# Kernel optimization log

Hardware: AMD Instinct MI355X
Metric: run time of the kernel (lower is better)

Reference implementation:

```python
import jax, jax.numpy as jnp
import numpy as np

NUM_HEADS = 16
HEAD_DIM = 128
HIDDEN = NUM_HEADS * HEAD_DIM


def rotate_half(x):
    x1, x2 = jnp.split(x, 2, axis=-1)
    return jnp.concatenate((-x2, x1), axis=-1)


def setup_inputs() -> dict:
    key = jax.random.key(0)
    ks = jax.random.split(key, 7)
    b, s = 2, 2048
    return {
        "hidden_states": jax.random.normal(ks[0], (b, s, HIDDEN), dtype=jnp.float32),
        "cos": jax.random.normal(ks[1], (1, 1, s, HEAD_DIM), dtype=jnp.float32),
        "sin": jax.random.normal(ks[2], (1, 1, s, HEAD_DIM), dtype=jnp.float32),
        "Wq": jax.random.normal(ks[3], (HIDDEN, HIDDEN), dtype=jnp.float32) * 0.02,
        "Wk": jax.random.normal(ks[4], (HIDDEN, HIDDEN), dtype=jnp.float32) * 0.02,
        "Wv": jax.random.normal(ks[5], (HIDDEN, HIDDEN), dtype=jnp.float32) * 0.02,
        "Wo": jax.random.normal(ks[6], (HIDDEN, HIDDEN), dtype=jnp.float32) * 0.02,
    }


def reference(hidden_states, cos, sin, Wq, Wk, Wv, Wo):
    b, s, _ = hidden_states.shape

    def proj(W):
        # [b,s,hidden] -> [b,H,s,D]
        return (hidden_states @ W).reshape(b, s, NUM_HEADS, HEAD_DIM).transpose(0, 2, 1, 3)

    q = proj(Wq)
    k = proj(Wk)
    v = proj(Wv)

    # RoPE: cos/sin [1,1,s,D] broadcast over batch and heads
    q = q * cos + rotate_half(q) * sin
    k = k * cos + rotate_half(k) * sin

    scale = 1.0 / jnp.sqrt(jnp.asarray(HEAD_DIM, dtype=q.dtype))
    scores = jnp.einsum("bhqd,bhkd->bhqk", q, k) * scale  # [b,H,s,s]
    attn = jax.nn.softmax(scores, axis=-1)  # no mask applied (matches source)
    out = jnp.einsum("bhqk,bhkd->bhqd", attn, v)  # [b,H,s,D]
    out = out.transpose(0, 2, 1, 3).reshape(b, s, HIDDEN)
    return out @ Wo
```

## Files before the change

### kernel.cpp

```cpp
#include <hip/hip_runtime.h>

typedef short bf16x8 __attribute__((ext_vector_type(8)));
typedef float f32x4 __attribute__((ext_vector_type(4)));

#define HID   2048
#define S_LEN 2048
#define NH    16
#define HD    128
#define BATCH 2
#define NROWS (BATCH * S_LEN)

__device__ __forceinline__ float bf2f(unsigned short u) {
    union { unsigned int i; float f; } v;
    v.i = ((unsigned int)u) << 16;
    return v.f;
}
__device__ __forceinline__ unsigned short f2bf(float f) {
    union { float f; unsigned int i; } v;
    v.f = f;
    unsigned int u = v.i;
    return (unsigned short)((u + 0x7fffu + ((u >> 16) & 1u)) >> 16);
}

__device__ __forceinline__ unsigned int pkbf(float a, float b) {
#if defined(__has_builtin) && __has_builtin(__builtin_amdgcn_cvt_pk_bf16_f32)
    typedef __bf16 bf2_t __attribute__((ext_vector_type(2)));
    bf2_t v = __builtin_amdgcn_cvt_pk_bf16_f32(a, b);
    unsigned int u;
    __builtin_memcpy(&u, &v, 4);
    return u;
#else
    return (unsigned int)f2bf(a) | ((unsigned int)f2bf(b) << 16);
#endif
}

__device__ __forceinline__ float exp2_fast(float x) {
#if defined(__has_builtin) && __has_builtin(__builtin_amdgcn_exp2f)
    return __builtin_amdgcn_exp2f(x);
#else
    return __expf(x * 0.6931471805599453f);
#endif
}

__device__ __forceinline__ void async16(const unsigned short* g, unsigned short* l) {
    __builtin_amdgcn_global_load_lds(
        (const __attribute__((address_space(1))) unsigned int*)g,
        (__attribute__((address_space(3))) unsigned int*)l, 16, 0, 0);
}

__global__ __launch_bounds__(256) void prep(const float* __restrict__ hs,
                                            const float* __restrict__ Wa,
                                            const float* __restrict__ Wb,
                                            const float* __restrict__ Wc,
                                            unsigned short* __restrict__ Xb,
                                            unsigned short* __restrict__ WT) {
    int z = blockIdx.z;
    int t = threadIdx.x;
    if (z == 3) {
        size_t idx = (((size_t)blockIdx.y * 64 + blockIdx.x) * 256 + t) * 8;
        float4 v0 = *(const float4*)(hs + idx);
        float4 v1 = *(const float4*)(hs + idx + 4);
        uint4 o;
        o.x = pkbf(v0.x, v0.y);
        o.y = pkbf(v0.z, v0.w);
        o.z = pkbf(v1.x, v1.y);
        o.w = pkbf(v1.z, v1.w);
        *(uint4*)(Xb + idx) = o;
        return;
    }
    __shared__ float tile[32][33];
    int tx = t & 31, ty = t >> 5;
    int bx = blockIdx.x, by = blockIdx.y;
    const float* W = (z == 0) ? Wa : ((z == 1) ? Wb : Wc);
    unsigned short* dst = WT + (size_t)z * HID * HID;
#pragma unroll
    for (int i = 0; i < 4; i++)
        tile[ty + i * 8][tx] = W[(size_t)(by * 32 + ty + i * 8) * HID + bx * 32 + tx];
    __syncthreads();
#pragma unroll
    for (int i = 0; i < 4; i++)
        dst[(size_t)(bx * 32 + ty + i * 8) * HID + by * 32 + tx] = f2bf(tile[tx][ty + i * 8]);
}

__global__ __launch_bounds__(256) void transpose_cast(const float* __restrict__ W,
                                                      unsigned short* __restrict__ WT) {
    __shared__ float tile[32][33];
    int t = threadIdx.x;
    int tx = t & 31, ty = t >> 5;
    int bx = blockIdx.x, by = blockIdx.y;
#pragma unroll
    for (int i = 0; i < 4; i++)
        tile[ty + i * 8][tx] = W[(size_t)(by * 32 + ty + i * 8) * HID + bx * 32 + tx];
    __syncthreads();
#pragma unroll
    for (int i = 0; i < 4; i++)
        WT[(size_t)(bx * 32 + ty + i * 8) * HID + by * 32 + tx] = f2bf(tile[tx][ty + i * 8]);
}

template <int MODE>
__global__ __launch_bounds__(256, 2) void gemm_bt(const unsigned short* __restrict__ A,
                                                  const unsigned short* __restrict__ Bt,
                                                  unsigned short* __restrict__ Qo,
                                                  unsigned short* __restrict__ Ko,
                                                  unsigned short* __restrict__ Vo,
                                                  float* __restrict__ Fo,
                                                  const float* __restrict__ cosp,
                                                  const float* __restrict__ sinp,
                                                  int n_shift) {
    __shared__ unsigned short SM[16384];
    unsigned short* Asm = SM;
    unsigned short* Bsm = SM + 8192;
    int t = threadIdx.x;
    int wave = t >> 6, lane = t & 63;
    int wm = wave >> 1, wn = wave & 1;
    int c = lane & 15, quad = lane >> 4;
    int m0 = blockIdx.y * 128, nloc = blockIdx.x * 128;

    int lr = lane >> 3;
    int cb = (lane & 7) ^ (lr & 7);
    const unsigned short* Ag = A + (size_t)(m0 + wave * 32 + lr) * HID + cb * 8;
    const unsigned short* Bg = Bt + (size_t)(nloc + wave * 32 + lr) * HID + cb * 8;
    unsigned short* Al = Asm + wave * 2048;
    unsigned short* Bl = Bsm + wave * 2048;

    f32x4 zero = {0.f, 0.f, 0.f, 0.f};
    f32x4 acc[4][4];
#pragma unroll
    for (int i = 0; i < 4; i++)
#pragma unroll
        for (int j = 0; j < 4; j++) acc[i][j] = zero;

    for (int it = 0; it < 32; it++) {
        int k0 = it * 64;
#pragma unroll
        for (int j = 0; j < 4; j++) {
            async16(Ag + k0 + j * 8 * HID, Al + j * 512);
            async16(Bg + k0 + j * 8 * HID, Bl + j * 512);
        }
        __syncthreads();
#pragma unroll
        for (int kk = 0; kk < 2; kk++) {
            bf16x8 af[4], bfr[4];
#pragma unroll
            for (int mt = 0; mt < 4; mt++)
                af[mt] = *(const bf16x8*)(Asm + (wm * 64 + mt * 16 + c) * 64 +
                                          (((kk * 4 + quad) ^ (c & 7)) * 8));
#pragma unroll
            for (int nt = 0; nt < 4; nt++)
                bfr[nt] = *(const bf16x8*)(Bsm + (wn * 64 + nt * 16 + c) * 64 +
                                           (((kk * 4 + quad) ^ (c & 7)) * 8));
#pragma unroll
            for (int mt = 0; mt < 4; mt++)
#pragma unroll
                for (int nt = 0; nt < 4; nt++)
                    acc[mt][nt] = __builtin_amdgcn_mfma_f32_16x16x32_bf16(af[mt], bfr[nt],
                                                                          acc[mt][nt], 0, 0, 0);
        }
        __syncthreads();
    }

    if (MODE == 2) {
#pragma unroll
        for (int mt = 0; mt < 4; mt++)
#pragma unroll
            for (int nt = 0; nt < 4; nt++)
#pragma unroll
                for (int r = 0; r < 4; r++) {
                    int row = m0 + wm * 64 + mt * 16 + quad * 4 + r;
                    int col = nloc + wn * 64 + nt * 16 + c;
                    Fo[(size_t)row * HID + col] = acc[mt][nt][r];
                }
    } else {
        int nglob0 = n_shift + nloc;
        int mat = nglob0 >> 11;
        int h = (nglob0 & 2047) >> 7;
        if (mat == 2) {
#pragma unroll
            for (int mt = 0; mt < 4; mt++)
#pragma unroll
                for (int nt = 0; nt < 4; nt++) {
                    int d = wn * 64 + nt * 16 + c;
                    int row0 = m0 + wm * 64 + mt * 16 + quad * 4;
                    int b = row0 >> 11, s = row0 & 2047;
                    ushort4 o;
                    o.x = f2bf(acc[mt][nt][0]);
                    o.y = f2bf(acc[mt][nt][1]);
                    o.z = f2bf(acc[mt][nt][2]);
                    o.w = f2bf(acc[mt][nt][3]);
                    *(ushort4*)(Vo + ((size_t)(b * NH + h) * HD + d) * S_LEN + s) = o;
                }
        } else {
            unsigned short* Cb = (mat == 0) ? Qo : Ko;
            float scl = (mat == 0) ? 0.12751743f : 1.0f;
            __syncthreads();
#pragma unroll
            for (int mt = 0; mt < 4; mt++)
#pragma unroll
                for (int nt = 0; nt < 4; nt++) {
                    ushort4 o;
                    o.x = f2bf(acc[mt][nt][0]);
                    o.y = f2bf(acc[mt][nt][1]);
                    o.z = f2bf(acc[mt][nt][2]);
                    o.w = f2bf(acc[mt][nt][3]);
                    *(ushort4*)(SM + (mt * 4 + nt) * 1024 + t * 4) = o;
                }
            __syncthreads();
            int partner = (wm * 2 + (wn ^ 1)) * 64 + lane;
            float sgn = wn ? 1.0f : -1.0f;
#pragma unroll
            for (int mt = 0; mt < 4; mt++) {
#pragma unroll
                for (int nt = 0; nt < 4; nt++) {
                    ushort4 pv = *(const ushort4*)(SM + (mt * 4 + nt) * 1024 + partner * 4);
                    float part[4] = {bf2f(pv.x), bf2f(pv.y), bf2f(pv.z), bf2f(pv.w)};
                    int col = wn * 64 + nt * 16 + c;
#pragma unroll
                    for (int r = 0; r < 4; r++) {
                        int row = m0 + wm * 64 + mt * 16 + quad * 4 + r;
                        int b = row >> 11, s = row & 2047;
                        float cv = cosp[s * HD + col], sv = sinp[s * HD + col];
                        float out = (acc[mt][nt][r] * cv + sgn * part[r] * sv) * scl;
                        Cb[((size_t)(b * NH + h) * S_LEN + s) * HD + col] = f2bf(out);
                    }
                }
            }
        }
    }
}

#define PKS 72
__global__ __launch_bounds__(256, 2) void attn_kernel(const unsigned short* __restrict__ Q,
                                                      const unsigned short* __restrict__ Kg,
                                                      const unsigned short* __restrict__ Vt,
                                                      unsigned short* __restrict__ Aout) {
    __shared__ unsigned short Ksm[2 * 64 * 128];
    __shared__ unsigned short Vsm[128 * 64];
    __shared__ __align__(16) unsigned short Psm[4 * 2 * 16 * PKS];
    int bh = blockIdx.y;
    int b = bh >> 4, h = bh & 15;
    int t = threadIdx.x;
    int wave = t >> 6, lane = t & 63;
    int c = lane & 15, quad = lane >> 4;
    int q0 = blockIdx.x * 128 + wave * 32;
    const unsigned short* Qp = Q + (size_t)bh * S_LEN * HD;
    const unsigned short* Kp = Kg + (size_t)bh * S_LEN * HD;
    const unsigned short* Vp = Vt + (size_t)bh * HD * S_LEN;

    bf16x8 qf[2][4];
#pragma unroll
    for (int qn = 0; qn < 2; qn++)
#pragma unroll
        for (int kk = 0; kk < 4; kk++)
            qf[qn][kk] = *(const bf16x8*)(Qp + (size_t)(q0 + qn * 16 + c) * HD + kk * 32 + quad * 8);

    f32x4 zero = {0.f, 0.f, 0.f, 0.f};
    f32x4 o_acc[2][8];
#pragma unroll
    for (int qn = 0; qn < 2; qn++)
#pragma unroll
        for (int nt = 0; nt < 8; nt++) o_acc[qn][nt] = zero;
    float lsum[2] = {0.f, 0.f};

#define STAGE_K(CH, BUF) {                                                      \
    _Pragma("unroll")                                                           \
    for (int j = 0; j < 4; j++) {                                               \
        int fc = (wave * 4 + j) * 64 + lane;                                    \
        int rK = fc >> 4, cbK = (fc & 15) ^ (rK & 15);                          \
        async16(Kp + (size_t)((CH) * 64 + rK) * HD + cbK * 8,                   \
                Ksm + (BUF) * 8192 + (wave * 4 + j) * 512); } }
#define STAGE_V(CH) {                                                           \
    _Pragma("unroll")                                                           \
    for (int j = 0; j < 4; j++) {                                               \
        int fc = (wave * 4 + j) * 64 + lane;                                    \
        int rV = fc >> 3, cbV = (fc & 7) ^ (rV & 7);                            \
        async16(Vp + (size_t)rV * S_LEN + (CH) * 64 + cbV * 8,                  \
                Vsm + (wave * 4 + j) * 512); } }

    STAGE_K(0, 0);
    STAGE_V(0);
    STAGE_K(1, 1);

    for (int i = 0; i < 32; i++) {
        const unsigned short* Kb = Ksm + (i & 1) * 8192;
        __builtin_amdgcn_s_waitcnt(0x0F78);
        __builtin_amdgcn_s_barrier();
        __builtin_amdgcn_sched_barrier(0);

        f32x4 sacc[4][2];
#pragma unroll
        for (int km = 0; km < 4; km++)
#pragma unroll
            for (int qn = 0; qn < 2; qn++) sacc[km][qn] = zero;
#pragma unroll
        for (int kk = 0; kk < 4; kk++) {
            bf16x8 kfr[4];
#pragma unroll
            for (int km = 0; km < 4; km++)
                kfr[km] = *(const bf16x8*)(Kb + (km * 16 + c) * HD + (((kk * 4 + quad) ^ c)) * 8);
#pragma unroll
            for (int km = 0; km < 4; km++)
#pragma unroll
                for (int qn = 0; qn < 2; qn++)
                    sacc[km][qn] = __builtin_amdgcn_mfma_f32_16x16x32_bf16(kfr[km], qf[qn][kk],
                                                                           sacc[km][qn], 0, 0, 0);
        }

#pragma unroll
        for (int qn = 0; qn < 2; qn++) {
#pragma unroll
            for (int km = 0; km < 4; km++) {
                float e0 = exp2_fast(sacc[km][qn][0]);
                float e1 = exp2_fast(sacc[km][qn][1]);
                float e2 = exp2_fast(sacc[km][qn][2]);
                float e3 = exp2_fast(sacc[km][qn][3]);
                lsum[qn] += (e0 + e1) + (e2 + e3);
                uint2 pk;
                pk.x = pkbf(e0, e1);
                pk.y = pkbf(e2, e3);
                *(uint2*)(Psm + ((wave * 2 + qn) * 16 + c) * PKS + km * 16 + quad * 4) = pk;
            }
        }
        asm volatile("" ::: "memory");
        __builtin_amdgcn_s_waitcnt(0xc07f);
        asm volatile("" ::: "memory");

        __builtin_amdgcn_sched_barrier(0);
        __builtin_amdgcn_s_waitcnt(0x0F74);
        __builtin_amdgcn_s_barrier();
        __builtin_amdgcn_sched_barrier(0);

#pragma unroll
        for (int kf = 0; kf < 2; kf++) {
            bf16x8 pf[2];
#pragma unroll
            for (int qn = 0; qn < 2; qn++)
                pf[qn] = *(const bf16x8*)(Psm + ((wave * 2 + qn) * 16 + c) * PKS + kf * 32 + quad * 8);
#pragma unroll
            for (int nt = 0; nt < 8; nt++) {
                bf16x8 vf = *(const bf16x8*)(Vsm + (nt * 16 + c) * 64 +
                                             (((kf * 4 + quad) ^ (c & 7))) * 8);
#pragma unroll
                for (int qn = 0; qn < 2; qn++)
                    o_acc[qn][nt] = __builtin_amdgcn_mfma_f32_16x16x32_bf16(pf[qn], vf,
                                                                            o_acc[qn][nt], 0, 0, 0);
            }
        }
        __builtin_amdgcn_sched_barrier(0);
        __builtin_amdgcn_s_barrier();
        __builtin_amdgcn_sched_barrier(0);

        int nv = (i + 1 > 31) ? 31 : i + 1;
        int nk = (i + 2 > 31) ? 31 : i + 2;
        STAGE_V(nv);
        STAGE_K(nk, (i & 1));
    }
#undef STAGE_K
#undef STAGE_V

#pragma unroll
    for (int qn = 0; qn < 2; qn++) {
        lsum[qn] += __shfl_xor(lsum[qn], 16);
        lsum[qn] += __shfl_xor(lsum[qn], 32);
    }
    float inv[2][4];
#pragma unroll
    for (int qn = 0; qn < 2; qn++)
#pragma unroll
        for (int r = 0; r < 4; r++)
            inv[qn][r] = 1.0f / __shfl(lsum[qn], quad * 4 + r);

#pragma unroll
    for (int qn = 0; qn < 2; qn++) {
#pragma unroll
        for (int r = 0; r < 4; r++) {
            int srow = q0 + qn * 16 + quad * 4 + r;
            size_t base = ((size_t)(b * S_LEN + srow)) * HID + h * HD;
#pragma unroll
            for (int nt = 0; nt < 8; nt++)
                Aout[base + nt * 16 + c] = f2bf(o_acc[qn][nt][r] * inv[qn][r]);
        }
    }
}

extern "C" void kernel_launch(void* const* d_in, const int* in_sizes, int n_in,
                              void* d_out, int out_size, void* d_ws, size_t ws_size,
                              hipStream_t stream) {
    const float* hs   = (const float*)d_in[0];
    const float* cosp = (const float*)d_in[1];
    const float* sinp = (const float*)d_in[2];
    const float* Wq   = (const float*)d_in[3];
    const float* Wk   = (const float*)d_in[4];
    const float* Wv   = (const float*)d_in[5];
    const float* Wo   = (const float*)d_in[6];

    char* ws = (char*)d_ws;
    unsigned short* Xb = (unsigned short*)(ws);
    unsigned short* Qb = (unsigned short*)(ws + (16ull << 20));
    unsigned short* Kb = (unsigned short*)(ws + (32ull << 20));
    unsigned short* Vb = (unsigned short*)(ws + (48ull << 20));
    unsigned short* WT = (unsigned short*)(ws + (64ull << 20));

    const bool fused = ws_size >= (88ull << 20);

    if (fused) {
        prep<<<dim3(64, 64, 4), 256, 0, stream>>>(hs, Wq, Wk, Wv, Xb, WT);
        gemm_bt<0><<<dim3(48, 32), 256, 0, stream>>>(Xb, WT, Qb, Kb, Vb, nullptr,
                                                     cosp, sinp, 0);
        attn_kernel<<<dim3(16, 32), 256, 0, stream>>>(Qb, Kb, Vb, Xb );
        unsigned short* WoT = (unsigned short*)(ws + (16ull << 20));
        transpose_cast<<<dim3(64, 64), 256, 0, stream>>>(Wo, WoT);
        gemm_bt<2><<<dim3(16, 32), 256, 0, stream>>>(Xb, WoT, nullptr, nullptr, nullptr,
                                                     (float*)d_out, cosp, sinp, 0);
    } else {
        prep<<<dim3(64, 64, 1), 256, 0, stream>>>(hs, Wq, Wq, Wq, Xb, WT);
        prep<<<dim3(64, 64, 4), 256, 0, stream>>>(hs, Wq, Wq, Wq, Xb, WT);
        gemm_bt<0><<<dim3(16, 32), 256, 0, stream>>>(Xb, WT, Qb, Kb, Vb, nullptr,
                                                     cosp, sinp, 0);
        transpose_cast<<<dim3(64, 64), 256, 0, stream>>>(Wk, WT);
        gemm_bt<0><<<dim3(16, 32), 256, 0, stream>>>(Xb, WT, Qb, Kb, Vb, nullptr,
                                                     cosp, sinp, 2048);
        transpose_cast<<<dim3(64, 64), 256, 0, stream>>>(Wv, WT);
        gemm_bt<0><<<dim3(16, 32), 256, 0, stream>>>(Xb, WT, Qb, Kb, Vb, nullptr,
                                                     cosp, sinp, 4096);
        attn_kernel<<<dim3(16, 32), 256, 0, stream>>>(Qb, Kb, Vb, Xb );
        transpose_cast<<<dim3(64, 64), 256, 0, stream>>>(Wo, WT);
        gemm_bt<2><<<dim3(16, 32), 256, 0, stream>>>(Xb, WT, nullptr, nullptr, nullptr,
                                                     (float*)d_out, cosp, sinp, 0);
    }
}
```

Before: 387.8 us.

## Widen weight transpose tiles, swizzle GEMM blocks across XCDs, raise MFMA priority

The weight transpose/cast kernels now process 64x32 tiles and write packed pairs of bf16 values as 32-bit stores, halving the block count and widening global stores. The GEMM remaps block indices so consecutive workgroups assigned to the same XCD share neighbouring tiles, aiming for better L2 reuse. The attention kernel raises wave priority around the MFMA loops to favour matrix issue over other waves. The hidden-state cast is split over two z slices to match the new grid shape.

```diff
diff --git a/kernel.cpp b/kernel.cpp
--- a/kernel.cpp
+++ b/kernel.cpp
@@ -56,8 +56,9 @@
                                             unsigned short* __restrict__ WT) {
     int z = blockIdx.z;
     int t = threadIdx.x;
-    if (z == 3) {
-        size_t idx = (((size_t)blockIdx.y * 64 + blockIdx.x) * 256 + t) * 8;
+    if (z >= 3) {
+        size_t blk = (size_t)(z - 3) * 2048 + blockIdx.y * 64 + blockIdx.x;
+        size_t idx = (blk * 256 + t) * 8;
         float4 v0 = *(const float4*)(hs + idx);
         float4 v1 = *(const float4*)(hs + idx + 4);
         uint4 o;
@@ -68,33 +69,41 @@
         *(uint4*)(Xb + idx) = o;
         return;
     }
-    __shared__ float tile[32][33];
+    __shared__ float tile[64][33];
     int tx = t & 31, ty = t >> 5;
     int bx = blockIdx.x, by = blockIdx.y;
     const float* W = (z == 0) ? Wa : ((z == 1) ? Wb : Wc);
     unsigned short* dst = WT + (size_t)z * HID * HID;
 #pragma unroll
-    for (int i = 0; i < 4; i++)
-        tile[ty + i * 8][tx] = W[(size_t)(by * 32 + ty + i * 8) * HID + bx * 32 + tx];
+    for (int i = 0; i < 8; i++)
+        tile[ty + i * 8][tx] = W[(size_t)(by * 64 + ty + i * 8) * HID + bx * 32 + tx];
     __syncthreads();
-#pragma unroll
-    for (int i = 0; i < 4; i++)
-        dst[(size_t)(bx * 32 + ty + i * 8) * HID + by * 32 + tx] = f2bf(tile[tx][ty + i * 8]);
+    int k2 = tx * 2;
+#pragma unroll
+    for (int i = 0; i < 4; i++) {
+        int j = ty + i * 8;
+        *(unsigned int*)(dst + (size_t)(bx * 32 + j) * HID + by * 64 + k2) =
+            pkbf(tile[k2][j], tile[k2 + 1][j]);
+    }
 }
 
 __global__ __launch_bounds__(256) void transpose_cast(const float* __restrict__ W,
                                                       unsigned short* __restrict__ WT) {
-    __shared__ float tile[32][33];
+    __shared__ float tile[64][33];
     int t = threadIdx.x;
     int tx = t & 31, ty = t >> 5;
     int bx = blockIdx.x, by = blockIdx.y;
 #pragma unroll
-    for (int i = 0; i < 4; i++)
-        tile[ty + i * 8][tx] = W[(size_t)(by * 32 + ty + i * 8) * HID + bx * 32 + tx];
+    for (int i = 0; i < 8; i++)
+        tile[ty + i * 8][tx] = W[(size_t)(by * 64 + ty + i * 8) * HID + bx * 32 + tx];
     __syncthreads();
-#pragma unroll
-    for (int i = 0; i < 4; i++)
-        WT[(size_t)(bx * 32 + ty + i * 8) * HID + by * 32 + tx] = f2bf(tile[tx][ty + i * 8]);
+    int k2 = tx * 2;
+#pragma unroll
+    for (int i = 0; i < 4; i++) {
+        int j = ty + i * 8;
+        *(unsigned int*)(WT + (size_t)(bx * 32 + j) * HID + by * 64 + k2) =
+            pkbf(tile[k2][j], tile[k2 + 1][j]);
+    }
 }
 
 template <int MODE>
@@ -114,7 +123,13 @@
     int wave = t >> 6, lane = t & 63;
     int wm = wave >> 1, wn = wave & 1;
     int c = lane & 15, quad = lane >> 4;
-    int m0 = blockIdx.y * 128, nloc = blockIdx.x * 128;
+
+    int nbx = gridDim.x;
+    int nwg = nbx * gridDim.y;
+    int bid = blockIdx.y * nbx + blockIdx.x;
+    int wg = (bid & 7) * (nwg >> 3) + (bid >> 3);
+    int bxx = wg % nbx, byy = wg / nbx;
+    int m0 = byy * 128, nloc = bxx * 128;
 
     int lr = lane >> 3;
     int cb = (lane & 7) ^ (lr & 7);
@@ -291,6 +306,7 @@
         for (int km = 0; km < 4; km++)
 #pragma unroll
             for (int qn = 0; qn < 2; qn++) sacc[km][qn] = zero;
+        __builtin_amdgcn_s_setprio(1);
 #pragma unroll
         for (int kk = 0; kk < 4; kk++) {
             bf16x8 kfr[4];
@@ -304,6 +320,7 @@
                     sacc[km][qn] = __builtin_amdgcn_mfma_f32_16x16x32_bf16(kfr[km], qf[qn][kk],
                                                                            sacc[km][qn], 0, 0, 0);
         }
+        __builtin_amdgcn_s_setprio(0);
 
 #pragma unroll
         for (int qn = 0; qn < 2; qn++) {
@@ -329,6 +346,7 @@
         __builtin_amdgcn_s_barrier();
         __builtin_amdgcn_sched_barrier(0);
 
+        __builtin_amdgcn_s_setprio(1);
 #pragma unroll
         for (int kf = 0; kf < 2; kf++) {
             bf16x8 pf[2];
@@ -345,6 +363,7 @@
                                                                             o_acc[qn][nt], 0, 0, 0);
             }
         }
+        __builtin_amdgcn_s_setprio(0);
         __builtin_amdgcn_sched_barrier(0);
         __builtin_amdgcn_s_barrier();
         __builtin_amdgcn_sched_barrier(0);
@@ -403,27 +422,26 @@
     const bool fused = ws_size >= (88ull << 20);
 
     if (fused) {
-        prep<<<dim3(64, 64, 4), 256, 0, stream>>>(hs, Wq, Wk, Wv, Xb, WT);
+        prep<<<dim3(64, 32, 5), 256, 0, stream>>>(hs, Wq, Wk, Wv, Xb, WT);
         gemm_bt<0><<<dim3(48, 32), 256, 0, stream>>>(Xb, WT, Qb, Kb, Vb, nullptr,
                                                      cosp, sinp, 0);
         attn_kernel<<<dim3(16, 32), 256, 0, stream>>>(Qb, Kb, Vb, Xb );
         unsigned short* WoT = (unsigned short*)(ws + (16ull << 20));
-        transpose_cast<<<dim3(64, 64), 256, 0, stream>>>(Wo, WoT);
+        transpose_cast<<<dim3(64, 32), 256, 0, stream>>>(Wo, WoT);
         gemm_bt<2><<<dim3(16, 32), 256, 0, stream>>>(Xb, WoT, nullptr, nullptr, nullptr,
                                                      (float*)d_out, cosp, sinp, 0);
     } else {
-        prep<<<dim3(64, 64, 1), 256, 0, stream>>>(hs, Wq, Wq, Wq, Xb, WT);
-        prep<<<dim3(64, 64, 4), 256, 0, stream>>>(hs, Wq, Wq, Wq, Xb, WT);
+        prep<<<dim3(64, 32, 5), 256, 0, stream>>>(hs, Wq, Wq, Wq, Xb, WT);
         gemm_bt<0><<<dim3(16, 32), 256, 0, stream>>>(Xb, WT, Qb, Kb, Vb, nullptr,
                                                      cosp, sinp, 0);
-        transpose_cast<<<dim3(64, 64), 256, 0, stream>>>(Wk, WT);
+        transpose_cast<<<dim3(64, 32), 256, 0, stream>>>(Wk, WT);
         gemm_bt<0><<<dim3(16, 32), 256, 0, stream>>>(Xb, WT, Qb, Kb, Vb, nullptr,
                                                      cosp, sinp, 2048);
-        transpose_cast<<<dim3(64, 64), 256, 0, stream>>>(Wv, WT);
+        transpose_cast<<<dim3(64, 32), 256, 0, stream>>>(Wv, WT);
         gemm_bt<0><<<dim3(16, 32), 256, 0, stream>>>(Xb, WT, Qb, Kb, Vb, nullptr,
                                                      cosp, sinp, 4096);
         attn_kernel<<<dim3(16, 32), 256, 0, stream>>>(Qb, Kb, Vb, Xb );
-        transpose_cast<<<dim3(64, 64), 256, 0, stream>>>(Wo, WT);
+        transpose_cast<<<dim3(64, 32), 256, 0, stream>>>(Wo, WT);
         gemm_bt<2><<<dim3(16, 32), 256, 0, stream>>>(Xb, WT, nullptr, nullptr, nullptr,
                                                      (float*)d_out, cosp, sinp, 0);
     }
```

After: 400.1 us. 3.2% more time.
